# Kernel tuning notes

Measured on AMD Instinct MI355X. Metric: run time of the kernel, lower is better.

Reference implementation:

```python
import jax, jax.numpy as jnp
import numpy as np

N = 6144; D0 = 512; D1 = 256; D2 = 128; K = 10
ALPHA = 1.0; BETA = 1.0; P = 0.004  # edge density -> ~25 avg degree


def _xavier(key, shape):
    limit = float(np.sqrt(6.0 / (shape[0] + shape[1])))
    return jax.random.uniform(key, shape, jnp.float32, -limit, limit)


def setup_inputs() -> dict:
    key = jax.random.key(0)
    ks = jax.random.split(key, 20)

    def adj(k):
        k1, k2 = jax.random.split(k)
        u = jax.random.uniform(k1, (N, N), jnp.float32)
        w = jax.random.uniform(k2, (N, N), jnp.float32)
        return jnp.where(u < P, w, 0.0)  # sparse weighted adjacency, dense storage

    return {
        "A": adj(ks[0]), "A2": adj(ks[1]),
        "X": jax.random.normal(ks[2], (N, D0), jnp.float32),
        "X2": jax.random.normal(ks[3], (N, D0), jnp.float32),
        "W11": _xavier(ks[4], (D0, D1)), "v111": _xavier(ks[5], (D1, 1)), "v112": _xavier(ks[6], (D1, 1)),
        "W12": _xavier(ks[7], (D1, D2)), "v121": _xavier(ks[8], (D2, 1)), "v122": _xavier(ks[9], (D2, 1)),
        "W21": _xavier(ks[10], (D0, D1)), "v211": _xavier(ks[11], (D1, 1)), "v212": _xavier(ks[12], (D1, 1)),
        "W22": _xavier(ks[13], (D1, D2)), "v221": _xavier(ks[14], (D2, 1)), "v222": _xavier(ks[15], (D2, 1)),
        "mu": _xavier(ks[16], (K, D2)),
    }


def _gat(A, H, v1, v2):
    # logits_ij = A_ij * (H v1)_i + A_ij * (H v2)_j, support = nonzeros of A;
    # torch.sparse.softmax over each row of sigmoid(logits) restricted to support.
    f1 = H @ v1                       # [N,1]
    f2 = H @ v2                       # [N,1]
    logits = A * f1 + A * f2.T        # [N,N]
    mask = A != 0.0
    e = jnp.where(mask, jnp.exp(jax.nn.sigmoid(logits)), 0.0)
    denom = jnp.sum(e, axis=1, keepdims=True)
    return e / jnp.where(denom == 0.0, 1.0, denom)  # empty rows -> all-zero row


def _autoenc(A, X, layers):
    H = X
    Cs = []
    for (W, v1, v2) in layers:          # encoder
        H = H @ W
        C = _gat(A, H, v1, v2)
        Cs.append(C)
        H = C @ H
    H_enc = H
    for i in range(len(layers) - 1, -1, -1):  # decoder (tied weights, cached attention)
        H = H @ layers[i][0].T
        H = Cs[i] @ H
    return H_enc, H


def reference(A, X, A2, X2, W11, v111, v112, W12, v121, v122,
              W21, v211, v212, W22, v221, v222, mu):
    H, X_ = _autoenc(A, X, [(W11, v111, v112), (W12, v121, v122)])
    H2, X_2 = _autoenc(A2, X2, [(W21, v211, v212), (W22, v221, v222)])
    H_F = H + H2 * BETA
    # Student-t soft assignment
    d2 = jnp.sum((H_F[:, None, :] - mu[None, :, :]) ** 2, axis=2)  # [N,K]
    q = (1.0 / (1.0 + d2 / ALPHA)) ** ((ALPHA + 1.0) / 2.0)
    q = q / jnp.sum(q, axis=1, keepdims=True)
    return (H_F, q, H, H2, X_, X_2)
```

## Files before the change

### kernel.cpp

```cpp
#include <hip/hip_runtime.h>
#include <hip/hip_bf16.h>

#define NN 6144
#define CAP 128

typedef short bf8 __attribute__((ext_vector_type(8)));
typedef float f4 __attribute__((ext_vector_type(4)));

__device__ inline unsigned short f2bf(float x) {
  union { float f; unsigned u; } v; v.f = x;
  unsigned r = v.u + 0x7fff + ((v.u >> 16) & 1);
  return (unsigned short)(r >> 16);
}
__device__ inline float bf2f(unsigned short b) {
  union { float f; unsigned u; } v; v.u = ((unsigned)b) << 16;
  return v.f;
}


__device__ void dev_sparsify(int bid, int tid,
    const float* __restrict__ A0, const float* __restrict__ A1,
    int* __restrict__ colsB, float* __restrict__ valsB, int* __restrict__ cntB) {
  const int br = bid >= 1536;
  const int bb = br ? bid - 1536 : bid;
  const float* __restrict__ A = br ? A1 : A0;
  int* cols = colsB + (size_t)br * NN * CAP;
  float* vals = valsB + (size_t)br * NN * CAP;
  int* cnt = cntB + br * NN;
  int row = (bb * 256 + tid) >> 6;
  int lane = tid & 63;
  const f4* __restrict__ arow = (const f4*)(A + (size_t)row * NN);
  int base = 0;
  for (int it = 0; it < 24; it += 6) {
    f4 v[6];
#pragma unroll
    for (int u = 0; u < 6; ++u) v[u] = __builtin_nontemporal_load(&arow[(it + u) * 64 + lane]);
#pragma unroll
    for (int u = 0; u < 6; ++u) {
      float xs[4] = {v[u][0], v[u][1], v[u][2], v[u][3]};
      unsigned long long m[4];
#pragma unroll
      for (int q = 0; q < 4; ++q) m[q] = __ballot(xs[q] != 0.0f);
      int off0 = base;
      int off1 = off0 + __popcll(m[0]);
      int off2 = off1 + __popcll(m[1]);
      int off3 = off2 + __popcll(m[2]);
      base = off3 + __popcll(m[3]);
      int offs[4] = {off0, off1, off2, off3};
      unsigned long long lmask = (1ull << lane) - 1ull;
#pragma unroll
      for (int q = 0; q < 4; ++q) {
        if (xs[q] != 0.0f) {
          int idx = offs[q] + __popcll(m[q] & lmask);
          if (idx < CAP) {
            cols[row * CAP + idx] = ((it + u) * 64 + lane) * 4 + q;
            vals[row * CAP + idx] = xs[q];
          }
        }
      }
    }
  }
  if (lane == 0) cnt[row] = base < CAP ? base : CAP;
}

__device__ void dev_convw(int cb, int tid,
    const float* __restrict__ W11, const float* __restrict__ W21,
    const float* __restrict__ W12, const float* __restrict__ W22,
    short* __restrict__ W1h, short* __restrict__ W1l,
    short* __restrict__ W1th, short* __restrict__ W1tl,
    short* __restrict__ W2h, short* __restrict__ W2l,
    short* __restrict__ W2th, short* __restrict__ W2tl) {
  const int S1 = 512 * 256, S2 = 256 * 128;
  int i = cb * 256 + tid;
  if (i < 2 * S1) {
    int br = i >= S1;
    int idx = br ? i - S1 : i;
    float x = (br ? W21 : W11)[idx];
    unsigned short h = f2bf(x), l = f2bf(x - bf2f(h));
    int r = idx / 256, c = idx % 256;
    size_t o = (size_t)br * S1;
    W1h[o + idx] = (short)h; W1l[o + idx] = (short)l;
    W1th[o + c * 512 + r] = (short)h; W1tl[o + c * 512 + r] = (short)l;
  } else {
    int i2 = i - 2 * S1;
    if (i2 >= 2 * S2) return;
    int br = i2 >= S2;
    int idx = br ? i2 - S2 : i2;
    float x = (br ? W22 : W12)[idx];
    unsigned short h = f2bf(x), l = f2bf(x - bf2f(h));
    int r = idx / 128, c = idx % 128;
    size_t o = (size_t)br * S2;
    W2h[o + idx] = (short)h; W2l[o + idx] = (short)l;
    W2th[o + c * 256 + r] = (short)h; W2tl[o + c * 256 + r] = (short)l;
  }
}

__device__ void dev_convX(int xb, int tid,
    const float* __restrict__ X0, const float* __restrict__ X1,
    short* __restrict__ XhB) {
  const int br = xb >= 3072;
  const int b = br ? xb - 3072 : xb;
  const float* __restrict__ in = br ? X1 : X0;
  short* hi = XhB + (size_t)br * NN * 512;
  int i = b * 256 + tid;
  float4 v = *(const float4*)&in[i * 4];
  short4 h;
  h.x = (short)f2bf(v.x);
  h.y = (short)f2bf(v.y);
  h.z = (short)f2bf(v.z);
  h.w = (short)f2bf(v.w);
  *(short4*)&hi[i * 4] = h;
}

__device__ void dev_fvec256(int fb, int tid,
    const short* __restrict__ HB, const float* __restrict__ v10,
    const float* __restrict__ v20, const float* __restrict__ v11,
    const float* __restrict__ v21, float* __restrict__ f1B, float* __restrict__ f2B) {
  const int br = fb >= 1536;
  const int bb = br ? fb - 1536 : fb;
  const short* H = HB + (size_t)br * NN * 256;
  const float* v1 = br ? v11 : v10;
  const float* v2 = br ? v21 : v20;
  float* f1 = f1B + br * NN;
  float* f2 = f2B + br * NN;
  int row = (bb * 256 + tid) >> 6;
  int lane = tid & 63;
  const short* hp = H + (size_t)row * 256 + lane * 4;
  float s1 = 0.f, s2 = 0.f;
#pragma unroll
  for (int e = 0; e < 4; ++e) {
    float h = bf2f((unsigned short)hp[e]);
    s1 += h * v1[lane * 4 + e];
    s2 += h * v2[lane * 4 + e];
  }
#pragma unroll
  for (int o = 32; o; o >>= 1) {
    s1 += __shfl_xor(s1, o);
    s2 += __shfl_xor(s2, o);
  }
  if (lane == 0) { f1[row] = s1; f2[row] = s2; }
}

#define GS 40
#define MFMA_BF16 __builtin_amdgcn_mfma_f32_16x16x32_bf16

template <bool ALO, int EPI>
__device__ void dev_gemm(int bx, int by, int br, int tid,
    const short* __restrict__ AhB, const short* __restrict__ AlB, size_t sA,
    const short* __restrict__ BhB, const short* __restrict__ BlB, size_t sB,
    float* __restrict__ CfB, short* __restrict__ ChB, short* __restrict__ ClB,
    size_t sC, int K, int Nn) {
  __shared__ short sAh[64 * GS], sBh[64 * GS], sBl[64 * GS];
  __shared__ short sAl[ALO ? 64 * GS : 64];
  const short* Ahg = AhB + br * sA;
  const short* Bhg = BhB + br * sB;
  const short* Blg = BlB + br * sB;
  const int bm = bx * 64, bn = by * 64;
  const int t = tid;
  const int lane = t & 63, w = t >> 6;
  const int wm = (w & 1) * 32, wn = (w >> 1) * 32;
  const int fr = lane & 15, fq = lane >> 4;
  const int srow = t >> 2, sk = (t & 3) * 8;

  f4 acc[2][2] = {};

  for (int k0 = 0; k0 < K; k0 += 32) {
    const size_t aoff = (size_t)(bm + srow) * K + k0 + sk;
    const size_t boff = (size_t)(bn + srow) * K + k0 + sk;
    bf8 vah = *(const bf8*)&Ahg[aoff];
    bf8 vbh = *(const bf8*)&Bhg[boff];
    bf8 vbl = *(const bf8*)&Blg[boff];
    bf8 val_;
    if constexpr (ALO) val_ = *(const bf8*)&(AlB + br * sA)[aoff];
    __syncthreads();
    *(bf8*)&sAh[srow * GS + sk] = vah;
    *(bf8*)&sBh[srow * GS + sk] = vbh;
    *(bf8*)&sBl[srow * GS + sk] = vbl;
    if constexpr (ALO) *(bf8*)&sAl[srow * GS + sk] = val_;
    __syncthreads();

    bf8 ah[2], al[2], bh[2], bl[2];
#pragma unroll
    for (int i = 0; i < 2; ++i) {
      ah[i] = *(bf8*)&sAh[(wm + i * 16 + fr) * GS + fq * 8];
      bh[i] = *(bf8*)&sBh[(wn + i * 16 + fr) * GS + fq * 8];
      bl[i] = *(bf8*)&sBl[(wn + i * 16 + fr) * GS + fq * 8];
      if constexpr (ALO) al[i] = *(bf8*)&sAl[(wm + i * 16 + fr) * GS + fq * 8];
    }
#pragma unroll
    for (int mi = 0; mi < 2; ++mi)
#pragma unroll
      for (int ni = 0; ni < 2; ++ni) {
        acc[mi][ni] = MFMA_BF16(ah[mi], bh[ni], acc[mi][ni], 0, 0, 0);
        acc[mi][ni] = MFMA_BF16(ah[mi], bl[ni], acc[mi][ni], 0, 0, 0);
        if constexpr (ALO) acc[mi][ni] = MFMA_BF16(al[mi], bh[ni], acc[mi][ni], 0, 0, 0);
      }
  }

  float* Cf = CfB ? CfB + br * sC : nullptr;
  short* Ch = ChB ? ChB + br * sC : nullptr;
  short* Cl = ClB ? ClB + br * sC : nullptr;
#pragma unroll
  for (int mi = 0; mi < 2; ++mi)
#pragma unroll
    for (int ni = 0; ni < 2; ++ni) {
      int cidx = bn + wn + ni * 16 + fr;
#pragma unroll
      for (int r = 0; r < 4; ++r) {
        size_t off = (size_t)(bm + wm + mi * 16 + fq * 4 + r) * Nn + cidx;
        float x = acc[mi][ni][r];
        if constexpr (EPI == 0) Cf[off] = x;
        if constexpr (EPI >= 1) {
          unsigned short h = f2bf(x);
          Ch[off] = (short)h;
          if constexpr (EPI == 2) Cl[off] = (short)f2bf(x - bf2f(h));
        }
      }
    }
}

__device__ void dev_spmm128(int sb, int tid,
    const int* __restrict__ colsB, const float* __restrict__ cvalsB,
    const int* __restrict__ cntB, const short* __restrict__ HinB,
    short* __restrict__ HhB) {
  const int br = sb >= 1536;
  const int bb = br ? sb - 1536 : sb;
  const int* cols = colsB + (size_t)br * NN * CAP;
  const float* cvals = cvalsB + (size_t)br * NN * CAP;
  const int* cnt = cntB + br * NN;
  const short* Hin = HinB + (size_t)br * NN * 128;
  int row = (bb * 256 + tid) >> 6;
  int lane = tid & 63;
  int c = cnt[row];
  const int base = row * CAP;
  float cv0 = 0.f, cv1 = 0.f;
  int j0 = 0, j1 = 0;
  if (lane < c) { j0 = cols[base + lane]; cv0 = cvals[base + lane]; }
  if (64 + lane < c) { j1 = cols[base + 64 + lane]; cv1 = cvals[base + 64 + lane]; }
  float2 acc = make_float2(0.f, 0.f);
  for (int k = 0; k < c; k += 4) {
    unsigned hv[4]; float cv[4];
#pragma unroll
    for (int u = 0; u < 4; ++u) {
      int kk = k + u;
      if (kk < c) {
        int jj = (kk & 64) ? j1 : j0;
        float cc = (kk & 64) ? cv1 : cv0;
        int j = __shfl(jj, kk & 63);
        cv[u] = __shfl(cc, kk & 63);
        hv[u] = *(const unsigned*)&Hin[(size_t)j * 128 + lane * 2];
      }
    }
#pragma unroll
    for (int u = 0; u < 4; ++u) {
      if (k + u < c) {
        acc.x += cv[u] * bf2f((unsigned short)(hv[u] & 0xffff));
        acc.y += cv[u] * bf2f((unsigned short)(hv[u] >> 16));
      }
    }
  }
  size_t o = (size_t)br * NN * 128 + (size_t)row * 128 + lane * 2;
  unsigned hw = (unsigned)(unsigned short)f2bf(acc.x) | ((unsigned)f2bf(acc.y) << 16);
  *(unsigned*)&HhB[o] = hw;
}

__device__ void dev_final(int fb, int tid,
    const float* __restrict__ H1e, const float* __restrict__ H2e,
    const float* __restrict__ mu, float* __restrict__ hf_out,
    float* __restrict__ q_out) {
  int row = (fb * 256 + tid) >> 6;
  int lane = tid & 63;
  float2 h1 = *(const float2*)&H1e[row * 128 + lane * 2];
  float2 h2 = *(const float2*)&H2e[row * 128 + lane * 2];
  float2 hf = make_float2(h1.x + h2.x, h1.y + h2.y);
  *(float2*)&hf_out[row * 128 + lane * 2] = hf;
  float d2[10];
#pragma unroll
  for (int k = 0; k < 10; ++k) {
    float dx = hf.x - mu[k * 128 + lane * 2];
    float dy = hf.y - mu[k * 128 + lane * 2 + 1];
    d2[k] = dx * dx + dy * dy;
  }
#pragma unroll
  for (int k = 0; k < 10; ++k)
#pragma unroll
    for (int o = 32; o; o >>= 1) d2[k] += __shfl_xor(d2[k], o);
  float q[10], s = 0.f;
#pragma unroll
  for (int k = 0; k < 10; ++k) { q[k] = 1.f / (1.f + d2[k]); s += q[k]; }
  float inv = 1.f / s;
  if (lane < 10) q_out[row * 10 + lane] = q[lane] * inv;
}


__global__ __launch_bounds__(256) void k1_prep(
    const float* A0, const float* A1, int* colsB, float* valsB, int* cntB,
    const float* W11, const float* W21, const float* W12, const float* W22,
    short* W1h, short* W1l, short* W1th, short* W1tl,
    short* W2h, short* W2l, short* W2th, short* W2tl,
    const float* X0, const float* X1, short* XhB) {
  int bid = blockIdx.x, tid = threadIdx.x;
  if (bid < 3072) dev_sparsify(bid, tid, A0, A1, colsB, valsB, cntB);
  else if (bid < 4352) dev_convw(bid - 3072, tid, W11, W21, W12, W22,
                                 W1h, W1l, W1th, W1tl, W2h, W2l, W2th, W2tl);
  else dev_convX(bid - 4352, tid, X0, X1, XhB);
}

template <bool ALO, int EPI>
__global__ __launch_bounds__(256) void gemm_nt(
    const short* AhB, const short* AlB, size_t sA,
    const short* BhB, const short* BlB, size_t sB,
    float* CfB, short* ChB, short* ClB, size_t sC, int K, int Nn) {
  dev_gemm<ALO, EPI>(blockIdx.x, blockIdx.y, blockIdx.z, threadIdx.x,
                     AhB, AlB, sA, BhB, BlB, sB, CfB, ChB, ClB, sC, K, Nn);
}

__global__ __launch_bounds__(256) void k3_gemm2_fvec(
    const short* H1h, const short* W2th, const short* W2tl, short* G1h,
    const float* v111, const float* v112, const float* v211, const float* v212,
    float* f1, float* f2) {
  int bid = blockIdx.x, tid = threadIdx.x;
  if (bid < 384) {
    int bx = bid % 96, r = bid / 96;
    int by = r & 1, br = r >> 1;
    dev_gemm<false, 1>(bx, by, br, tid, H1h, nullptr, (size_t)NN * 256,
                       W2th, W2tl, (size_t)256 * 128, nullptr, G1h, nullptr,
                       (size_t)NN * 128, 256, 128);
  } else {
    dev_fvec256(bid - 384, tid, H1h, v111, v112, v211, v212, f1, f2);
  }
}

template <bool WF32, bool FUSE>
__global__ __launch_bounds__(256) void gatspmm_kernel(
    const int* __restrict__ colsB, const float* __restrict__ avalsB,
    const int* __restrict__ cntB, const float* __restrict__ f1B,
    const float* __restrict__ f2B, float* __restrict__ cvalsB,
    const short* __restrict__ HinB, float* __restrict__ HoutB,
    short* __restrict__ HhB,
    const float* __restrict__ nv10, const float* __restrict__ nv20,
    const float* __restrict__ nv11, const float* __restrict__ nv21,
    float* __restrict__ g1B, float* __restrict__ g2B) {
  const int br = blockIdx.y;
  const int* cols = colsB + (size_t)br * NN * CAP;
  const float* avals = avalsB + (size_t)br * NN * CAP;
  const int* cnt = cntB + br * NN;
  const float* f1 = f1B + br * NN;
  const float* f2 = f2B + br * NN;
  float* cvals = cvalsB + (size_t)br * NN * CAP;
  const short* Hin = HinB + (size_t)br * NN * 128;
  int row = (blockIdx.x * blockDim.x + threadIdx.x) >> 6;
  int lane = threadIdx.x & 63;
  int c = cnt[row];
  float f1i = f1[row];
  const int base = row * CAP;
  float e0 = 0.f, e1 = 0.f;
  int j0 = 0, j1 = 0;
  {
    int k = lane;
    if (k < c) {
      float a = avals[base + k];
      j0 = cols[base + k];
      float lg = a * (f1i + f2[j0]);
      e0 = expf(1.f / (1.f + expf(-lg)));
    }
    k = 64 + lane;
    if (k < c) {
      float a = avals[base + k];
      j1 = cols[base + k];
      float lg = a * (f1i + f2[j1]);
      e1 = expf(1.f / (1.f + expf(-lg)));
    }
  }
  float s = e0 + e1;
#pragma unroll
  for (int o = 32; o; o >>= 1) s += __shfl_xor(s, o);
  float inv = (s == 0.f) ? 1.f : 1.f / s;
  if (lane < c) cvals[base + lane] = e0 * inv;
  if (64 + lane < c) cvals[base + 64 + lane] = e1 * inv;

  float2 acc = make_float2(0.f, 0.f);
  for (int k = 0; k < c; k += 4) {
    unsigned hv[4]; float cv[4];
#pragma unroll
    for (int u = 0; u < 4; ++u) {
      int kk = k + u;
      if (kk < c) {
        int jj = (kk & 64) ? j1 : j0;
        float ee = (kk & 64) ? e1 : e0;
        int j = __shfl(jj, kk & 63);
        cv[u] = __shfl(ee, kk & 63) * inv;
        hv[u] = *(const unsigned*)&Hin[(size_t)j * 128 + lane * 2];
      }
    }
#pragma unroll
    for (int u = 0; u < 4; ++u) {
      if (k + u < c) {
        acc.x += cv[u] * bf2f((unsigned short)(hv[u] & 0xffff));
        acc.y += cv[u] * bf2f((unsigned short)(hv[u] >> 16));
      }
    }
  }
  size_t o = (size_t)br * NN * 128 + (size_t)row * 128 + lane * 2;
  if constexpr (WF32) *(float2*)&HoutB[o] = acc;
  unsigned hw = (unsigned)(unsigned short)f2bf(acc.x) | ((unsigned)f2bf(acc.y) << 16);
  *(unsigned*)&HhB[o] = hw;
  if constexpr (FUSE) {
    const float* w1 = br ? nv11 : nv10;
    const float* w2 = br ? nv21 : nv20;
    float s1 = acc.x * w1[lane * 2] + acc.y * w1[lane * 2 + 1];
    float s2 = acc.x * w2[lane * 2] + acc.y * w2[lane * 2 + 1];
#pragma unroll
    for (int o2 = 32; o2; o2 >>= 1) {
      s1 += __shfl_xor(s1, o2);
      s2 += __shfl_xor(s2, o2);
    }
    if (lane == 0) { g1B[br * NN + row] = s1; g2B[br * NN + row] = s2; }
  }
}

__global__ __launch_bounds__(256) void k6_spmm_final(
    const int* colsB, const float* c2v, const int* cntB,
    const short* Hech, short* C2sh,
    const float* H1e, const float* H2e, const float* mu,
    float* hf_out, float* q_out) {
  int bid = blockIdx.x, tid = threadIdx.x;
  if (bid < 3072) dev_spmm128(bid, tid, colsB, c2v, cntB, Hech, C2sh);
  else dev_final(bid - 3072, tid, H1e, H2e, mu, hf_out, q_out);
}

__global__ __launch_bounds__(256) void spmm128_kernel(
    const int* colsB, const float* cvalsB, const int* cntB,
    const short* HinB, short* HhB) {
  dev_spmm128(blockIdx.x + blockIdx.y * 1536, threadIdx.x, colsB, cvalsB, cntB, HinB, HhB);
}

extern "C" void kernel_launch(void* const* d_in, const int* in_sizes, int n_in,
                              void* d_out, int out_size, void* d_ws, size_t ws_size,
                              hipStream_t stream) {
  const int D0 = 512, D1 = 256, D2 = 128;
  const int S1 = D0 * D1, S2 = D1 * D2;
  float* out = (float*)d_out;
  const size_t o0 = 0;
  const size_t o1 = o0 + (size_t)NN * 128;
  const size_t o2 = o1 + (size_t)NN * 10;
  const size_t o3 = o2 + (size_t)NN * 128;
  const size_t o4 = o3 + (size_t)NN * 128;
  const size_t o5 = o4 + (size_t)NN * 512;

  char* w = (char*)d_ws;
  auto alloc = [&](size_t bytes) -> void* {
    void* p = (void*)w;
    w += (bytes + 255) & ~(size_t)255;
    return p;
  };
  int*   cols  = (int*)  alloc((size_t)2 * NN * CAP * 4);
  float* avals = (float*)alloc((size_t)2 * NN * CAP * 4);
  float* c1v   = (float*)alloc((size_t)2 * NN * CAP * 4);
  float* c2v   = (float*)alloc((size_t)2 * NN * CAP * 4);
  int*   cnt   = (int*)  alloc((size_t)2 * NN * 4);
  float* f1    = (float*)alloc((size_t)2 * NN * 4);
  float* f2    = (float*)alloc((size_t)2 * NN * 4);
  float* g1    = (float*)alloc((size_t)2 * NN * 4);
  float* g2    = (float*)alloc((size_t)2 * NN * 4);
  short* Xh    = (short*)alloc((size_t)2 * NN * D0 * 2);
  short* H1h   = (short*)alloc((size_t)2 * NN * D1 * 2);
  short* G1h   = (short*)alloc((size_t)2 * NN * D2 * 2);
  short* H2h   = (short*)alloc((size_t)2 * NN * D2 * 2);
  short* Hech  = (short*)alloc((size_t)2 * NN * D2 * 2);
  short* C2sh  = (short*)alloc((size_t)2 * NN * D2 * 2);
  short* Cth   = (short*)alloc((size_t)2 * NN * D2 * 2);
  short* Uh    = (short*)alloc((size_t)2 * NN * D1 * 2);
  short* Ul    = (short*)alloc((size_t)2 * NN * D1 * 2);
  short* W1h   = (short*)alloc((size_t)2 * S1 * 2);
  short* W1l   = (short*)alloc((size_t)2 * S1 * 2);
  short* W1th  = (short*)alloc((size_t)2 * S1 * 2);
  short* W1tl  = (short*)alloc((size_t)2 * S1 * 2);
  short* W2h   = (short*)alloc((size_t)2 * S2 * 2);
  short* W2l   = (short*)alloc((size_t)2 * S2 * 2);
  short* W2th  = (short*)alloc((size_t)2 * S2 * 2);
  short* W2tl  = (short*)alloc((size_t)2 * S2 * 2);

  const float* A   = (const float*)d_in[0];
  const float* A2  = (const float*)d_in[1];
  const float* X   = (const float*)d_in[2];
  const float* X2  = (const float*)d_in[3];
  const float* W11 = (const float*)d_in[4];
  const float* v111= (const float*)d_in[5];
  const float* v112= (const float*)d_in[6];
  const float* W12 = (const float*)d_in[7];
  const float* v121= (const float*)d_in[8];
  const float* v122= (const float*)d_in[9];
  const float* W21 = (const float*)d_in[10];
  const float* v211= (const float*)d_in[11];
  const float* v212= (const float*)d_in[12];
  const float* W22 = (const float*)d_in[13];
  const float* v221= (const float*)d_in[14];
  const float* v222= (const float*)d_in[15];
  const float* mu  = (const float*)d_in[16];

  const dim3 rows2(NN / 4, 2);

  k1_prep<<<10496, 256, 0, stream>>>(
      A, A2, cols, avals, cnt, W11, W21, W12, W22,
      W1h, W1l, W1th, W1tl, W2h, W2l, W2th, W2tl, X, X2, Xh);
  gemm_nt<false, 1><<<dim3(NN / 64, D1 / 64, 2), 256, 0, stream>>>(
      Xh, nullptr, (size_t)NN * D0, W1th, W1tl, (size_t)S1,
      nullptr, H1h, nullptr, (size_t)NN * D1, D0, D1);
  k3_gemm2_fvec<<<3456, 256, 0, stream>>>(
      H1h, W2th, W2tl, G1h, v111, v112, v211, v212, f1, f2);
  gatspmm_kernel<false, true><<<rows2, 256, 0, stream>>>(
      cols, avals, cnt, f1, f2, c1v, G1h, nullptr, H2h,
      v121, v122, v221, v222, g1, g2);
  gatspmm_kernel<true, false><<<rows2, 256, 0, stream>>>(
      cols, avals, cnt, g1, g2, c2v, H2h, out + o2, Hech,
      nullptr, nullptr, nullptr, nullptr, nullptr, nullptr);
  k6_spmm_final<<<4608, 256, 0, stream>>>(
      cols, c2v, cnt, Hech, C2sh, out + o2, out + o3, mu, out + o0, out + o1);
  spmm128_kernel<<<rows2, 256, 0, stream>>>(cols, c1v, cnt, C2sh, Cth);
  gemm_nt<false, 2><<<dim3(NN / 64, D1 / 64, 2), 256, 0, stream>>>(
      Cth, nullptr, (size_t)NN * D2, W2h, W2l, (size_t)S2,
      nullptr, Uh, Ul, (size_t)NN * D1, D2, D1);
  gemm_nt<true, 0><<<dim3(NN / 64, D0 / 64, 2), 256, 0, stream>>>(
      Uh, Ul, (size_t)NN * D1, W1h, W1l, (size_t)S1,
      out + o4, nullptr, nullptr, (size_t)NN * D0, D1, D0);
}
```

Before: 170.8 us.

## Co-schedule adjacency sparsify with first GEMM and stage rows through LDS

Splits the old prep kernel so weight/X conversion runs first. The dense-adjacency sparsify then shares one launch with the first layer GEMM, so the bandwidth-bound scan and the compute-bound GEMM can overlap. Sparsify now pulls each row half into LDS with direct global-to-LDS 16-byte loads before the ballot compaction. The SpMM gather loops are also unrolled from 4 to 8 to keep more loads in flight. This adds a 48KB static LDS buffer per block, which may lower occupancy for the fused kernel, and the extra launch adds a little overhead.

After: 183.2 us. +7.2%, slower.

```diff
diff --git a/kernel.cpp b/kernel.cpp
--- a/kernel.cpp
+++ b/kernel.cpp
@@ -17,8 +17,14 @@
   return v.f;
 }
 
-
-__device__ void dev_sparsify(int bid, int tid,
+__device__ inline void gload16(const float* g, void* l) {
+  __builtin_amdgcn_global_load_lds(
+      (const __attribute__((address_space(1))) void*)g,
+      (__attribute__((address_space(3))) void*)l, 16, 0, 0);
+}
+
+
+__device__ void dev_sparsify(int bid, int tid, char* smem,
     const float* __restrict__ A0, const float* __restrict__ A1,
     int* __restrict__ colsB, float* __restrict__ valsB, int* __restrict__ cntB) {
   const int br = bid >= 1536;
@@ -27,17 +33,23 @@
   int* cols = colsB + (size_t)br * NN * CAP;
   float* vals = valsB + (size_t)br * NN * CAP;
   int* cnt = cntB + br * NN;
-  int row = (bb * 256 + tid) >> 6;
-  int lane = tid & 63;
-  const f4* __restrict__ arow = (const f4*)(A + (size_t)row * NN);
+  const int wv = tid >> 6, lane = tid & 63;
+  const int row = bb * 4 + wv;
+  const float* __restrict__ arow = A + (size_t)row * NN;
+  char* buf = smem + wv * 12288;
   int base = 0;
-  for (int it = 0; it < 24; it += 6) {
-    f4 v[6];
-#pragma unroll
-    for (int u = 0; u < 6; ++u) v[u] = __builtin_nontemporal_load(&arow[(it + u) * 64 + lane]);
-#pragma unroll
-    for (int u = 0; u < 6; ++u) {
-      float xs[4] = {v[u][0], v[u][1], v[u][2], v[u][3]};
+  const int rbase = row * CAP;
+  for (int half = 0; half < 2; ++half) {
+#pragma unroll
+    for (int i = 0; i < 12; ++i)
+      gload16(arow + half * 3072 + i * 256 + lane * 4, buf + i * 1024);
+    asm volatile("s_waitcnt vmcnt(0)" ::: "memory");
+    __builtin_amdgcn_sched_barrier(0);
+#pragma unroll
+    for (int i = 0; i < 12; ++i) {
+      f4 v = *(f4*)(buf + i * 1024 + lane * 16);
+      const int it = half * 12 + i;
+      float xs[4] = {v[0], v[1], v[2], v[3]};
       unsigned long long m[4];
 #pragma unroll
       for (int q = 0; q < 4; ++q) m[q] = __ballot(xs[q] != 0.0f);
@@ -53,8 +65,8 @@
         if (xs[q] != 0.0f) {
           int idx = offs[q] + __popcll(m[q] & lmask);
           if (idx < CAP) {
-            cols[row * CAP + idx] = ((it + u) * 64 + lane) * 4 + q;
-            vals[row * CAP + idx] = xs[q];
+            cols[rbase + idx] = (it * 64 + lane) * 4 + q;
+            vals[rbase + idx] = xs[q];
           }
         }
       }
@@ -145,13 +157,15 @@
 #define MFMA_BF16 __builtin_amdgcn_mfma_f32_16x16x32_bf16
 
 template <bool ALO, int EPI>
-__device__ void dev_gemm(int bx, int by, int br, int tid,
+__device__ void dev_gemm(int bx, int by, int br, int tid, char* smemc,
     const short* __restrict__ AhB, const short* __restrict__ AlB, size_t sA,
     const short* __restrict__ BhB, const short* __restrict__ BlB, size_t sB,
     float* __restrict__ CfB, short* __restrict__ ChB, short* __restrict__ ClB,
     size_t sC, int K, int Nn) {
-  __shared__ short sAh[64 * GS], sBh[64 * GS], sBl[64 * GS];
-  __shared__ short sAl[ALO ? 64 * GS : 64];
+  short* sAh = (short*)smemc;
+  short* sBh = sAh + 64 * GS;
+  short* sBl = sBh + 64 * GS;
+  short* sAl = sBl + 64 * GS;
   const short* Ahg = AhB + br * sA;
   const short* Bhg = BhB + br * sB;
   const short* Blg = BlB + br * sB;
@@ -238,10 +252,10 @@
   if (lane < c) { j0 = cols[base + lane]; cv0 = cvals[base + lane]; }
   if (64 + lane < c) { j1 = cols[base + 64 + lane]; cv1 = cvals[base + 64 + lane]; }
   float2 acc = make_float2(0.f, 0.f);
-  for (int k = 0; k < c; k += 4) {
-    unsigned hv[4]; float cv[4];
-#pragma unroll
-    for (int u = 0; u < 4; ++u) {
+  for (int k = 0; k < c; k += 8) {
+    unsigned hv[8]; float cv[8];
+#pragma unroll
+    for (int u = 0; u < 8; ++u) {
       int kk = k + u;
       if (kk < c) {
         int jj = (kk & 64) ? j1 : j0;
@@ -252,7 +266,7 @@
       }
     }
 #pragma unroll
-    for (int u = 0; u < 4; ++u) {
+    for (int u = 0; u < 8; ++u) {
       if (k + u < c) {
         acc.x += cv[u] * bf2f((unsigned short)(hv[u] & 0xffff));
         acc.y += cv[u] * bf2f((unsigned short)(hv[u] >> 16));
@@ -293,17 +307,32 @@
 }
 
 
-__global__ __launch_bounds__(256) void k1_prep(
-    const float* A0, const float* A1, int* colsB, float* valsB, int* cntB,
+__global__ __launch_bounds__(256) void k0_prep(
     const float* W11, const float* W21, const float* W12, const float* W22,
     short* W1h, short* W1l, short* W1th, short* W1tl,
     short* W2h, short* W2l, short* W2th, short* W2tl,
     const float* X0, const float* X1, short* XhB) {
   int bid = blockIdx.x, tid = threadIdx.x;
-  if (bid < 3072) dev_sparsify(bid, tid, A0, A1, colsB, valsB, cntB);
-  else if (bid < 4352) dev_convw(bid - 3072, tid, W11, W21, W12, W22,
-                                 W1h, W1l, W1th, W1tl, W2h, W2l, W2th, W2tl);
-  else dev_convX(bid - 4352, tid, X0, X1, XhB);
+  if (bid < 1280) dev_convw(bid, tid, W11, W21, W12, W22,
+                            W1h, W1l, W1th, W1tl, W2h, W2l, W2th, W2tl);
+  else dev_convX(bid - 1280, tid, X0, X1, XhB);
+}
+
+__global__ __launch_bounds__(256) void k1_sparsify_gemm1(
+    const float* A0, const float* A1, int* colsB, float* valsB, int* cntB,
+    const short* Xh, const short* W1th, const short* W1tl, short* H1h) {
+  __shared__ char smem[49152];
+  int bid = blockIdx.x, tid = threadIdx.x;
+  if (bid < 3072) {
+    dev_sparsify(bid, tid, smem, A0, A1, colsB, valsB, cntB);
+  } else {
+    int g = bid - 3072;
+    int bx = g % 96, r = g / 96;
+    int by = r & 3, brz = r >> 2;
+    dev_gemm<false, 1>(bx, by, brz, tid, smem, Xh, nullptr, (size_t)NN * 512,
+                       W1th, W1tl, (size_t)512 * 256, nullptr, H1h, nullptr,
+                       (size_t)NN * 256, 512, 256);
+  }
 }
 
 template <bool ALO, int EPI>
@@ -311,7 +340,8 @@
     const short* AhB, const short* AlB, size_t sA,
     const short* BhB, const short* BlB, size_t sB,
     float* CfB, short* ChB, short* ClB, size_t sC, int K, int Nn) {
-  dev_gemm<ALO, EPI>(blockIdx.x, blockIdx.y, blockIdx.z, threadIdx.x,
+  __shared__ char smem[(ALO ? 4 : 3) * 64 * GS * 2];
+  dev_gemm<ALO, EPI>(blockIdx.x, blockIdx.y, blockIdx.z, threadIdx.x, smem,
                      AhB, AlB, sA, BhB, BlB, sB, CfB, ChB, ClB, sC, K, Nn);
 }
 
@@ -319,11 +349,12 @@
     const short* H1h, const short* W2th, const short* W2tl, short* G1h,
     const float* v111, const float* v112, const float* v211, const float* v212,
     float* f1, float* f2) {
+  __shared__ char smem[3 * 64 * GS * 2];
   int bid = blockIdx.x, tid = threadIdx.x;
   if (bid < 384) {
     int bx = bid % 96, r = bid / 96;
     int by = r & 1, br = r >> 1;
-    dev_gemm<false, 1>(bx, by, br, tid, H1h, nullptr, (size_t)NN * 256,
+    dev_gemm<false, 1>(bx, by, br, tid, smem, H1h, nullptr, (size_t)NN * 256,
                        W2th, W2tl, (size_t)256 * 128, nullptr, G1h, nullptr,
                        (size_t)NN * 128, 256, 128);
   } else {
@@ -380,10 +411,10 @@
   if (64 + lane < c) cvals[base + 64 + lane] = e1 * inv;
 
   float2 acc = make_float2(0.f, 0.f);
-  for (int k = 0; k < c; k += 4) {
-    unsigned hv[4]; float cv[4];
-#pragma unroll
-    for (int u = 0; u < 4; ++u) {
+  for (int k = 0; k < c; k += 8) {
+    unsigned hv[8]; float cv[8];
+#pragma unroll
+    for (int u = 0; u < 8; ++u) {
       int kk = k + u;
       if (kk < c) {
         int jj = (kk & 64) ? j1 : j0;
@@ -394,7 +425,7 @@
       }
     }
 #pragma unroll
-    for (int u = 0; u < 4; ++u) {
+    for (int u = 0; u < 8; ++u) {
       if (k + u < c) {
         acc.x += cv[u] * bf2f((unsigned short)(hv[u] & 0xffff));
         acc.y += cv[u] * bf2f((unsigned short)(hv[u] >> 16));
@@ -501,12 +532,10 @@
 
   const dim3 rows2(NN / 4, 2);
 
-  k1_prep<<<10496, 256, 0, stream>>>(
-      A, A2, cols, avals, cnt, W11, W21, W12, W22,
-      W1h, W1l, W1th, W1tl, W2h, W2l, W2th, W2tl, X, X2, Xh);
-  gemm_nt<false, 1><<<dim3(NN / 64, D1 / 64, 2), 256, 0, stream>>>(
-      Xh, nullptr, (size_t)NN * D0, W1th, W1tl, (size_t)S1,
-      nullptr, H1h, nullptr, (size_t)NN * D1, D0, D1);
+  k0_prep<<<7424, 256, 0, stream>>>(
+      W11, W21, W12, W22, W1h, W1l, W1th, W1tl, W2h, W2l, W2th, W2tl, X, X2, Xh);
+  k1_sparsify_gemm1<<<3840, 256, 0, stream>>>(
+      A, A2, cols, avals, cnt, Xh, W1th, W1tl, H1h);
   k3_gemm2_fvec<<<3456, 256, 0, stream>>>(
       H1h, W2th, W2tl, G1h, v111, v112, v211, v212, f1, f2);
   gatspmm_kernel<false, true><<<rows2, 256, 0, stream>>>(
```

## Fold decoder weights into a precomputed W1·W2 product, drop one GEMM

Applied to the files above, without the earlier changes.

The decoder computes (C1 @ H) @ W2^T @ W1^T. The change precomputes the combined weight Wc = W1 @ W2 (512x128) in fp32 inside the prep kernel, stored as bf16 hi/lo pairs. This removes one GEMM launch and the Uh/Ul intermediate, and shrinks the last GEMM's K from 256 to 128. To keep accuracy, the spmm now also writes a bf16 low part. Separately, the sparse gather loops are unrolled from 4 to 8, and GEMM shared memory is passed in as a pointer.

Result: faster. 164.3 us (-3.8%).

```diff
diff --git a/kernel.cpp b/kernel.cpp
--- a/kernel.cpp
+++ b/kernel.cpp
@@ -66,9 +66,7 @@
 __device__ void dev_convw(int cb, int tid,
     const float* __restrict__ W11, const float* __restrict__ W21,
     const float* __restrict__ W12, const float* __restrict__ W22,
-    short* __restrict__ W1h, short* __restrict__ W1l,
     short* __restrict__ W1th, short* __restrict__ W1tl,
-    short* __restrict__ W2h, short* __restrict__ W2l,
     short* __restrict__ W2th, short* __restrict__ W2tl) {
   const int S1 = 512 * 256, S2 = 256 * 128;
   int i = cb * 256 + tid;
@@ -79,7 +77,6 @@
     unsigned short h = f2bf(x), l = f2bf(x - bf2f(h));
     int r = idx / 256, c = idx % 256;
     size_t o = (size_t)br * S1;
-    W1h[o + idx] = (short)h; W1l[o + idx] = (short)l;
     W1th[o + c * 512 + r] = (short)h; W1tl[o + c * 512 + r] = (short)l;
   } else {
     int i2 = i - 2 * S1;
@@ -90,7 +87,6 @@
     unsigned short h = f2bf(x), l = f2bf(x - bf2f(h));
     int r = idx / 128, c = idx % 128;
     size_t o = (size_t)br * S2;
-    W2h[o + idx] = (short)h; W2l[o + idx] = (short)l;
     W2th[o + c * 256 + r] = (short)h; W2tl[o + c * 256 + r] = (short)l;
   }
 }
@@ -112,6 +108,58 @@
   *(short4*)&hi[i * 4] = h;
 }
 
+__device__ void dev_wc2(int wb, int tid, char* smemc,
+    const float* __restrict__ W11, const float* __restrict__ W12,
+    const float* __restrict__ W21, const float* __restrict__ W22,
+    short* __restrict__ Wch, short* __restrict__ Wcl) {
+  const int bx = wb & 7, by = (wb >> 3) & 1, br = wb >> 4;
+  const float* W1 = br ? W21 : W11;
+  const float* W2 = br ? W22 : W12;
+  short* Ch = Wch + (size_t)br * 512 * 128;
+  short* Cl = Wcl + (size_t)br * 512 * 128;
+  float (*As)[68] = (float(*)[68])smemc;
+  float (*Bs)[68] = (float(*)[68])(smemc + 16 * 68 * 4);
+  const int bm = bx * 64, bn = by * 64;
+  const int t = tid;
+  const int tm = (t >> 4) * 4, tn = (t & 15) * 4;
+  const int la_m = t >> 2, la_k = (t & 3) * 4;
+  const int lb_k = t >> 4, lb_n = (t & 15) * 4;
+  float acc[4][4] = {};
+  for (int k0 = 0; k0 < 256; k0 += 16) {
+    float4 a4 = *(const float4*)&W1[(size_t)(bm + la_m) * 256 + k0 + la_k];
+    float4 b4 = *(const float4*)&W2[(size_t)(k0 + lb_k) * 128 + bn + lb_n];
+    __syncthreads();
+    As[la_k + 0][la_m] = a4.x;
+    As[la_k + 1][la_m] = a4.y;
+    As[la_k + 2][la_m] = a4.z;
+    As[la_k + 3][la_m] = a4.w;
+    Bs[lb_k][lb_n + 0] = b4.x;
+    Bs[lb_k][lb_n + 1] = b4.y;
+    Bs[lb_k][lb_n + 2] = b4.z;
+    Bs[lb_k][lb_n + 3] = b4.w;
+    __syncthreads();
+#pragma unroll
+    for (int k = 0; k < 16; ++k) {
+      float a0 = As[k][tm + 0], a1 = As[k][tm + 1], a2 = As[k][tm + 2], a3 = As[k][tm + 3];
+      float b0 = Bs[k][tn + 0], b1 = Bs[k][tn + 1], b2 = Bs[k][tn + 2], b3 = Bs[k][tn + 3];
+      acc[0][0] += a0 * b0; acc[0][1] += a0 * b1; acc[0][2] += a0 * b2; acc[0][3] += a0 * b3;
+      acc[1][0] += a1 * b0; acc[1][1] += a1 * b1; acc[1][2] += a1 * b2; acc[1][3] += a1 * b3;
+      acc[2][0] += a2 * b0; acc[2][1] += a2 * b1; acc[2][2] += a2 * b2; acc[2][3] += a2 * b3;
+      acc[3][0] += a3 * b0; acc[3][1] += a3 * b1; acc[3][2] += a3 * b2; acc[3][3] += a3 * b3;
+    }
+  }
+#pragma unroll
+  for (int i = 0; i < 4; ++i)
+#pragma unroll
+    for (int j = 0; j < 4; ++j) {
+      float x = acc[i][j];
+      size_t off = (size_t)(bm + tm + i) * 128 + bn + tn + j;
+      unsigned short h = f2bf(x);
+      Ch[off] = (short)h;
+      Cl[off] = (short)f2bf(x - bf2f(h));
+    }
+}
+
 __device__ void dev_fvec256(int fb, int tid,
     const short* __restrict__ HB, const float* __restrict__ v10,
     const float* __restrict__ v20, const float* __restrict__ v11,
@@ -145,13 +193,15 @@
 #define MFMA_BF16 __builtin_amdgcn_mfma_f32_16x16x32_bf16
 
 template <bool ALO, int EPI>
-__device__ void dev_gemm(int bx, int by, int br, int tid,
+__device__ void dev_gemm(int bx, int by, int br, int tid, char* smemc,
     const short* __restrict__ AhB, const short* __restrict__ AlB, size_t sA,
     const short* __restrict__ BhB, const short* __restrict__ BlB, size_t sB,
     float* __restrict__ CfB, short* __restrict__ ChB, short* __restrict__ ClB,
     size_t sC, int K, int Nn) {
-  __shared__ short sAh[64 * GS], sBh[64 * GS], sBl[64 * GS];
-  __shared__ short sAl[ALO ? 64 * GS : 64];
+  short* sAh = (short*)smemc;
+  short* sBh = sAh + 64 * GS;
+  short* sBl = sBh + 64 * GS;
+  short* sAl = sBl + 64 * GS;
   const short* Ahg = AhB + br * sA;
   const short* Bhg = BhB + br * sB;
   const short* Blg = BlB + br * sB;
@@ -219,10 +269,11 @@
     }
 }
 
+template <bool WLO>
 __device__ void dev_spmm128(int sb, int tid,
     const int* __restrict__ colsB, const float* __restrict__ cvalsB,
     const int* __restrict__ cntB, const short* __restrict__ HinB,
-    short* __restrict__ HhB) {
+    short* __restrict__ HhB, short* __restrict__ HlB) {
   const int br = sb >= 1536;
   const int bb = br ? sb - 1536 : sb;
   const int* cols = colsB + (size_t)br * NN * CAP;
@@ -238,10 +289,10 @@
   if (lane < c) { j0 = cols[base + lane]; cv0 = cvals[base + lane]; }
   if (64 + lane < c) { j1 = cols[base + 64 + lane]; cv1 = cvals[base + 64 + lane]; }
   float2 acc = make_float2(0.f, 0.f);
-  for (int k = 0; k < c; k += 4) {
-    unsigned hv[4]; float cv[4];
-#pragma unroll
-    for (int u = 0; u < 4; ++u) {
+  for (int k = 0; k < c; k += 8) {
+    unsigned hv[8]; float cv[8];
+#pragma unroll
+    for (int u = 0; u < 8; ++u) {
       int kk = k + u;
       if (kk < c) {
         int jj = (kk & 64) ? j1 : j0;
@@ -252,7 +303,7 @@
       }
     }
 #pragma unroll
-    for (int u = 0; u < 4; ++u) {
+    for (int u = 0; u < 8; ++u) {
       if (k + u < c) {
         acc.x += cv[u] * bf2f((unsigned short)(hv[u] & 0xffff));
         acc.y += cv[u] * bf2f((unsigned short)(hv[u] >> 16));
@@ -260,8 +311,12 @@
     }
   }
   size_t o = (size_t)br * NN * 128 + (size_t)row * 128 + lane * 2;
-  unsigned hw = (unsigned)(unsigned short)f2bf(acc.x) | ((unsigned)f2bf(acc.y) << 16);
-  *(unsigned*)&HhB[o] = hw;
+  unsigned short hx = f2bf(acc.x), hy = f2bf(acc.y);
+  *(unsigned*)&HhB[o] = (unsigned)hx | ((unsigned)hy << 16);
+  if constexpr (WLO) {
+    unsigned short lx = f2bf(acc.x - bf2f(hx)), ly = f2bf(acc.y - bf2f(hy));
+    *(unsigned*)&HlB[o] = (unsigned)lx | ((unsigned)ly << 16);
+  }
 }
 
 __device__ void dev_final(int fb, int tid,
@@ -296,14 +351,16 @@
 __global__ __launch_bounds__(256) void k1_prep(
     const float* A0, const float* A1, int* colsB, float* valsB, int* cntB,
     const float* W11, const float* W21, const float* W12, const float* W22,
-    short* W1h, short* W1l, short* W1th, short* W1tl,
-    short* W2h, short* W2l, short* W2th, short* W2tl,
-    const float* X0, const float* X1, short* XhB) {
+    short* W1th, short* W1tl, short* W2th, short* W2tl,
+    const float* X0, const float* X1, short* XhB,
+    short* Wc2h, short* Wc2l) {
+  __shared__ char smem[2 * 16 * 68 * 4];
   int bid = blockIdx.x, tid = threadIdx.x;
   if (bid < 3072) dev_sparsify(bid, tid, A0, A1, colsB, valsB, cntB);
   else if (bid < 4352) dev_convw(bid - 3072, tid, W11, W21, W12, W22,
-                                 W1h, W1l, W1th, W1tl, W2h, W2l, W2th, W2tl);
-  else dev_convX(bid - 4352, tid, X0, X1, XhB);
+                                 W1th, W1tl, W2th, W2tl);
+  else if (bid < 10496) dev_convX(bid - 4352, tid, X0, X1, XhB);
+  else dev_wc2(bid - 10496, tid, smem, W11, W12, W21, W22, Wc2h, Wc2l);
 }
 
 template <bool ALO, int EPI>
@@ -311,7 +368,8 @@
     const short* AhB, const short* AlB, size_t sA,
     const short* BhB, const short* BlB, size_t sB,
     float* CfB, short* ChB, short* ClB, size_t sC, int K, int Nn) {
-  dev_gemm<ALO, EPI>(blockIdx.x, blockIdx.y, blockIdx.z, threadIdx.x,
+  __shared__ char smem[(ALO ? 4 : 3) * 64 * GS * 2];
+  dev_gemm<ALO, EPI>(blockIdx.x, blockIdx.y, blockIdx.z, threadIdx.x, smem,
                      AhB, AlB, sA, BhB, BlB, sB, CfB, ChB, ClB, sC, K, Nn);
 }
 
@@ -319,11 +377,12 @@
     const short* H1h, const short* W2th, const short* W2tl, short* G1h,
     const float* v111, const float* v112, const float* v211, const float* v212,
     float* f1, float* f2) {
+  __shared__ char smem[3 * 64 * GS * 2];
   int bid = blockIdx.x, tid = threadIdx.x;
   if (bid < 384) {
     int bx = bid % 96, r = bid / 96;
     int by = r & 1, br = r >> 1;
-    dev_gemm<false, 1>(bx, by, br, tid, H1h, nullptr, (size_t)NN * 256,
+    dev_gemm<false, 1>(bx, by, br, tid, smem, H1h, nullptr, (size_t)NN * 256,
                        W2th, W2tl, (size_t)256 * 128, nullptr, G1h, nullptr,
                        (size_t)NN * 128, 256, 128);
   } else {
@@ -380,10 +439,10 @@
   if (64 + lane < c) cvals[base + 64 + lane] = e1 * inv;
 
   float2 acc = make_float2(0.f, 0.f);
-  for (int k = 0; k < c; k += 4) {
-    unsigned hv[4]; float cv[4];
-#pragma unroll
-    for (int u = 0; u < 4; ++u) {
+  for (int k = 0; k < c; k += 8) {
+    unsigned hv[8]; float cv[8];
+#pragma unroll
+    for (int u = 0; u < 8; ++u) {
       int kk = k + u;
       if (kk < c) {
         int jj = (kk & 64) ? j1 : j0;
@@ -394,7 +453,7 @@
       }
     }
 #pragma unroll
-    for (int u = 0; u < 4; ++u) {
+    for (int u = 0; u < 8; ++u) {
       if (k + u < c) {
         acc.x += cv[u] * bf2f((unsigned short)(hv[u] & 0xffff));
         acc.y += cv[u] * bf2f((unsigned short)(hv[u] >> 16));
@@ -425,14 +484,15 @@
     const float* H1e, const float* H2e, const float* mu,
     float* hf_out, float* q_out) {
   int bid = blockIdx.x, tid = threadIdx.x;
-  if (bid < 3072) dev_spmm128(bid, tid, colsB, c2v, cntB, Hech, C2sh);
+  if (bid < 3072) dev_spmm128<false>(bid, tid, colsB, c2v, cntB, Hech, C2sh, nullptr);
   else dev_final(bid - 3072, tid, H1e, H2e, mu, hf_out, q_out);
 }
 
-__global__ __launch_bounds__(256) void spmm128_kernel(
+__global__ __launch_bounds__(256) void spmm128hl_kernel(
     const int* colsB, const float* cvalsB, const int* cntB,
-    const short* HinB, short* HhB) {
-  dev_spmm128(blockIdx.x + blockIdx.y * 1536, threadIdx.x, colsB, cvalsB, cntB, HinB, HhB);
+    const short* HinB, short* HhB, short* HlB) {
+  dev_spmm128<true>(blockIdx.x + blockIdx.y * 1536, threadIdx.x,
+                    colsB, cvalsB, cntB, HinB, HhB, HlB);
 }
 
 extern "C" void kernel_launch(void* const* d_in, const int* in_sizes, int n_in,
@@ -470,16 +530,13 @@
   short* Hech  = (short*)alloc((size_t)2 * NN * D2 * 2);
   short* C2sh  = (short*)alloc((size_t)2 * NN * D2 * 2);
   short* Cth   = (short*)alloc((size_t)2 * NN * D2 * 2);
-  short* Uh    = (short*)alloc((size_t)2 * NN * D1 * 2);
-  short* Ul    = (short*)alloc((size_t)2 * NN * D1 * 2);
-  short* W1h   = (short*)alloc((size_t)2 * S1 * 2);
-  short* W1l   = (short*)alloc((size_t)2 * S1 * 2);
+  short* Ctl   = (short*)alloc((size_t)2 * NN * D2 * 2);
   short* W1th  = (short*)alloc((size_t)2 * S1 * 2);
   short* W1tl  = (short*)alloc((size_t)2 * S1 * 2);
-  short* W2h   = (short*)alloc((size_t)2 * S2 * 2);
-  short* W2l   = (short*)alloc((size_t)2 * S2 * 2);
   short* W2th  = (short*)alloc((size_t)2 * S2 * 2);
   short* W2tl  = (short*)alloc((size_t)2 * S2 * 2);
+  short* Wc2h  = (short*)alloc((size_t)2 * 512 * 128 * 2);
+  short* Wc2l  = (short*)alloc((size_t)2 * 512 * 128 * 2);
 
   const float* A   = (const float*)d_in[0];
   const float* A2  = (const float*)d_in[1];
@@ -501,9 +558,9 @@
 
   const dim3 rows2(NN / 4, 2);
 
-  k1_prep<<<10496, 256, 0, stream>>>(
+  k1_prep<<<10528, 256, 0, stream>>>(
       A, A2, cols, avals, cnt, W11, W21, W12, W22,
-      W1h, W1l, W1th, W1tl, W2h, W2l, W2th, W2tl, X, X2, Xh);
+      W1th, W1tl, W2th, W2tl, X, X2, Xh, Wc2h, Wc2l);
   gemm_nt<false, 1><<<dim3(NN / 64, D1 / 64, 2), 256, 0, stream>>>(
       Xh, nullptr, (size_t)NN * D0, W1th, W1tl, (size_t)S1,
       nullptr, H1h, nullptr, (size_t)NN * D1, D0, D1);
@@ -517,11 +574,8 @@
       nullptr, nullptr, nullptr, nullptr, nullptr, nullptr);
   k6_spmm_final<<<4608, 256, 0, stream>>>(
       cols, c2v, cnt, Hech, C2sh, out + o2, out + o3, mu, out + o0, out + o1);
-  spmm128_kernel<<<rows2, 256, 0, stream>>>(cols, c1v, cnt, C2sh, Cth);
-  gemm_nt<false, 2><<<dim3(NN / 64, D1 / 64, 2), 256, 0, stream>>>(
-      Cth, nullptr, (size_t)NN * D2, W2h, W2l, (size_t)S2,
-      nullptr, Uh, Ul, (size_t)NN * D1, D2, D1);
+  spmm128hl_kernel<<<rows2, 256, 0, stream>>>(cols, c1v, cnt, C2sh, Cth, Ctl);
   gemm_nt<true, 0><<<dim3(NN / 64, D0 / 64, 2), 256, 0, stream>>>(
-      Uh, Ul, (size_t)NN * D1, W1h, W1l, (size_t)S1,
-      out + o4, nullptr, nullptr, (size_t)NN * D0, D1, D0);
-}
+      Cth, Ctl, (size_t)NN * D2, Wc2h, Wc2l, (size_t)(512 * 128),
+      out + o4, nullptr, nullptr, (size_t)NN * D0, D2, D0);
+}
```
